# Performance work log

Hardware: AMD Instinct MI355X
Metric: run time of the kernel (lower is better)

Reference implementation:

```python
import jax, jax.numpy as jnp
import numpy as np

D_K = 64

def setup_inputs() -> dict:
    key = jax.random.key(0)
    ks = jax.random.split(key, 9)
    B, S, D = 8, 2048, 512
    d_k, d_v = 64, 64
    return {
        "q_in": jax.random.normal(ks[0], (B, S, D), jnp.float32),
        "k_in": jax.random.normal(ks[1], (B, S, D), jnp.float32),
        "v_in": jax.random.normal(ks[2], (B, S, D), jnp.float32),
        "Wq": jax.random.normal(ks[3], (D, d_k), jnp.float32) * 0.05,
        "bq": jax.random.normal(ks[4], (d_k,), jnp.float32) * 0.05,
        "Wk": jax.random.normal(ks[5], (D, d_k), jnp.float32) * 0.05,
        "bk": jax.random.normal(ks[6], (d_k,), jnp.float32) * 0.05,
        "Wv": jax.random.normal(ks[7], (D, d_v), jnp.float32) * 0.05,
        "bv": jax.random.normal(ks[8], (d_v,), jnp.float32) * 0.05,
    }

def reference(q_in, k_in, v_in, Wq, bq, Wk, bk, Wv, bv):
    # Dense projections: x @ W + b
    q = jnp.einsum('bsd,dk->bsk', q_in, Wq) + bq  # [B,S,d_k]
    k = jnp.einsum('bsd,dk->bsk', k_in, Wk) + bk  # [B,S,d_k]
    v = jnp.einsum('bsd,dv->bsv', v_in, Wv) + bv  # [B,S,d_v]
    scale = 1.0 / np.sqrt(D_K).astype(np.float32)
    scores = jnp.einsum('bqk,bsk->bqs', q, k) * scale  # [B,S,S]
    attn = jax.nn.softmax(scores, axis=-1)
    return jnp.einsum('bqs,bsv->bqv', attn, v)  # [B,S,d_v]
```

## Files before the change

### kernel.cpp

```cpp
#include <hip/hip_runtime.h>
#include <hip/hip_bf16.h>
#include <cstdint>

typedef __attribute__((ext_vector_type(8))) short short8;
typedef __attribute__((ext_vector_type(16))) float f32x16;

#if __has_builtin(__builtin_amdgcn_exp2f)
#define EXP2F(x) __builtin_amdgcn_exp2f(x)
#else
#define EXP2F(x) exp2f(x)
#endif

#define MFMA32(A, B, C) __builtin_amdgcn_mfma_f32_32x32x16_bf16((A), (B), (C), 0, 0, 0)

__device__ __forceinline__ unsigned short f2bf(float f) {
  unsigned int u = __builtin_bit_cast(unsigned int, f);
  u += 0x7FFFu + ((u >> 16) & 1u);
  return (unsigned short)(u >> 16);
}

__global__ __launch_bounds__(256) void prep_wt(
    const float* __restrict__ Wq, const float* __restrict__ Wk,
    const float* __restrict__ Wv, unsigned short* __restrict__ Wt)
{
  int idx = blockIdx.x * 256 + threadIdx.x;
  int which = idx >> 15;
  int rem = idx & 32767;
  int n = rem >> 9;
  int k = rem & 511;
  const float* W = (which == 0) ? Wq : (which == 1) ? Wk : Wv;
  Wt[idx] = f2bf(W[k * 64 + n]);
}

__global__ __launch_bounds__(256, 3) void proj_kernel(
    const float* __restrict__ qin, const float* __restrict__ kin,
    const float* __restrict__ vin, const unsigned short* __restrict__ Wt,
    const float* __restrict__ bq, const float* __restrict__ bk,
    const float* __restrict__ bv,
    unsigned short* __restrict__ Qo, unsigned short* __restrict__ Ko,
    unsigned short* __restrict__ Vto)
{
  __shared__ unsigned short Xs[64 * 136];

  const int which = blockIdx.y;
  const float* X    = (which == 0) ? qin : (which == 1) ? kin : vin;
  const float* bias = (which == 0) ? bq  : (which == 1) ? bk  : bv;

  const int tid = threadIdx.x;
  const int lane = tid & 63, wv = tid >> 6;
  const int h = lane >> 5, l31 = lane & 31;
  const int grp = wv & 1, nh = wv >> 1;
  const int m0 = blockIdx.x * 64;

  const unsigned short* wcol =
      Wt + (size_t)which * 64 * 512 + (size_t)(nh * 32 + l31) * 512 + h * 8;

  const int srow = tid >> 5;
  const int skoff = tid & 31;
  const float* xg = X + (size_t)(m0 + srow) * 512 + skoff * 4;

  f32x16 acc = {};
  for (int c = 0; c < 4; ++c) {
    __syncthreads();
    #pragma unroll
    for (int j = 0; j < 8; ++j) {
      float4 a = *(const float4*)(xg + (size_t)(8 * j) * 512 + c * 128);
      unsigned int w0 = (unsigned int)f2bf(a.x) | ((unsigned int)f2bf(a.y) << 16);
      unsigned int w1 = (unsigned int)f2bf(a.z) | ((unsigned int)f2bf(a.w) << 16);
      uint2 pw; pw.x = w0; pw.y = w1;
      *(uint2*)(&Xs[(srow + 8 * j) * 136 + skoff * 4]) = pw;
    }
    __syncthreads();
    const unsigned short* arow = &Xs[(grp * 32 + l31) * 136 + h * 8];
    const unsigned short* wk = wcol + c * 128;
    #pragma unroll
    for (int ks = 0; ks < 8; ++ks) {
      short8 af = *(const short8*)(arow + ks * 16);
      short8 bf = *(const short8*)(wk + ks * 16);
      acc = MFMA32(af, bf, acc);
    }
  }

  const float bv0 = bias[nh * 32 + l31];

  if (which < 2) {
    const float scale = which ? 1.0f : 0.18033688f;
    unsigned short* Y = which ? Ko : Qo;
    #pragma unroll
    for (int r = 0; r < 16; ++r) {
      int row = (r & 3) + 8 * (r >> 2) + 4 * h;
      Y[(size_t)(m0 + grp * 32 + row) * 64 + nh * 32 + l31] =
          f2bf((acc[r] + bv0) * scale);
    }
  } else {
    __syncthreads();
    unsigned short* TB = Xs;
    #pragma unroll
    for (int r = 0; r < 16; ++r) {
      int row = (r & 3) + 8 * (r >> 2) + 4 * h;
      TB[(nh * 32 + l31) * 68 + grp * 32 + row] = f2bf(acc[r] + bv0);
    }
    __syncthreads();
    int bidx = blockIdx.x >> 5;
    int s0 = (blockIdx.x & 31) * 64;
    for (int i = tid; i < 64 * 16; i += 256) {
      int n = i >> 4, cs = i & 15;
      ushort4 v4 = *(const ushort4*)(TB + n * 68 + cs * 4);
      *(ushort4*)(Vto + ((size_t)bidx * 64 + n) * 2048 + s0 + cs * 4) = v4;
    }
  }
}

__global__ __launch_bounds__(512, 2) void attn_kernel(
    const unsigned short* __restrict__ Q, const unsigned short* __restrict__ K,
    const unsigned short* __restrict__ Vt, float* __restrict__ out)
{
  __shared__ float ObS[4][16][64];
  __shared__ float MpS[4][64];
  __shared__ float LpS[4][64];

  const int tid = threadIdx.x;
  const int lane = tid & 63, w = tid >> 6;
  const int h = lane >> 5, l31 = lane & 31;
  const int b = blockIdx.y;
  const int q0 = blockIdx.x * 64;

  short8 qf[2][4];
  #pragma unroll
  for (int qt = 0; qt < 2; ++qt) {
    const unsigned short* qp = Q + ((size_t)(b * 2048 + q0 + qt * 32 + l31)) * 64 + h * 8;
    #pragma unroll
    for (int c = 0; c < 4; ++c) qf[qt][c] = *(const short8*)(qp + c * 16);
  }

  f32x16 o00 = {}, o01 = {}, o10 = {}, o11 = {};
  float m0 = -1e30f, m1 = -1e30f, ls0 = 0.f, ls1 = 0.f;

  for (int st = 0; st < 8; ++st) {
    const int kb = w * 256 + st * 32;
    short8 kf[4];
    const unsigned short* kp = K + ((size_t)(b * 2048 + kb + l31)) * 64 + h * 8;
    #pragma unroll
    for (int c = 0; c < 4; ++c) kf[c] = *(const short8*)(kp + c * 16);
    short8 vf0[2], vf1[2];
    {
      const unsigned short* vp0 = Vt + ((size_t)(b * 64 + l31)) * 2048 + kb + h * 8;
      const unsigned short* vp1 = Vt + ((size_t)(b * 64 + 32 + l31)) * 2048 + kb + h * 8;
      vf0[0] = *(const short8*)(vp0);  vf0[1] = *(const short8*)(vp0 + 16);
      vf1[0] = *(const short8*)(vp1);  vf1[1] = *(const short8*)(vp1 + 16);
    }
    #pragma unroll
    for (int qt = 0; qt < 2; ++qt) {
      f32x16 sT = {};
      #pragma unroll
      for (int c = 0; c < 4; ++c) sT = MFMA32(kf[c], qf[qt][c], sT);
      float mx = sT[0];
      #pragma unroll
      for (int r = 1; r < 16; ++r) mx = fmaxf(mx, sT[r]);
      mx = fmaxf(mx, __shfl_xor(mx, 32, 64));
      float mold = qt ? m1 : m0;
      float mnew = fmaxf(mold, mx);
      float alpha = EXP2F(mold - mnew);
      float rs = 0.f;
      float p[16];
      #pragma unroll
      for (int r = 0; r < 16; ++r) { p[r] = EXP2F(sT[r] - mnew); rs += p[r]; }
      rs += __shfl_xor(rs, 32, 64);
      unsigned int pk[8];
      #pragma unroll
      for (int i = 0; i < 8; ++i)
        pk[i] = (unsigned int)f2bf(p[2 * i]) | ((unsigned int)f2bf(p[2 * i + 1]) << 16);
      unsigned int ex[8];
      #pragma unroll
      for (int i = 0; i < 8; ++i) ex[i] = (unsigned int)__shfl_xor((int)pk[i], 32, 64);
      uint4 cc0, cc1;
      if (h == 0) { cc0 = make_uint4(pk[0], pk[1], ex[0], ex[1]); cc1 = make_uint4(pk[4], pk[5], ex[4], ex[5]); }
      else        { cc0 = make_uint4(ex[2], ex[3], pk[2], pk[3]); cc1 = make_uint4(ex[6], ex[7], pk[6], pk[7]); }
      short8 P0 = __builtin_bit_cast(short8, cc0);
      short8 P1 = __builtin_bit_cast(short8, cc1);
      if (qt == 0) {
        m0 = mnew; ls0 = ls0 * alpha + rs;
        o00 *= alpha; o10 *= alpha;
        o00 = MFMA32(vf0[0], P0, o00); o00 = MFMA32(vf0[1], P1, o00);
        o10 = MFMA32(vf1[0], P0, o10); o10 = MFMA32(vf1[1], P1, o10);
      } else {
        m1 = mnew; ls1 = ls1 * alpha + rs;
        o01 *= alpha; o11 *= alpha;
        o01 = MFMA32(vf0[0], P0, o01); o01 = MFMA32(vf0[1], P1, o01);
        o11 = MFMA32(vf1[0], P0, o11); o11 = MFMA32(vf1[1], P1, o11);
      }
    }
  }

  for (int half = 4; half > 0; half >>= 1) {
    const bool writer = (w >= half) && (w < 2 * half);
    const bool merger = (w < half);
    __syncthreads();
    if (writer && h == 0) {
      MpS[w - half][l31] = m0;      LpS[w - half][l31] = ls0;
      MpS[w - half][32 + l31] = m1; LpS[w - half][32 + l31] = ls1;
    }
    __syncthreads();
    float fb0 = 0.f, fb1 = 0.f;
    if (merger) {
      float pm0 = MpS[w][l31],      pl0 = LpS[w][l31];
      float pm1 = MpS[w][32 + l31], pl1 = LpS[w][32 + l31];
      float nm0 = fmaxf(m0, pm0), nm1 = fmaxf(m1, pm1);
      float fa0 = EXP2F(m0 - nm0); fb0 = EXP2F(pm0 - nm0);
      float fa1 = EXP2F(m1 - nm1); fb1 = EXP2F(pm1 - nm1);
      m0 = nm0; m1 = nm1;
      ls0 = ls0 * fa0 + pl0 * fb0; ls1 = ls1 * fa1 + pl1 * fb1;
      o00 *= fa0; o10 *= fa0; o01 *= fa1; o11 *= fa1;
    }
    __syncthreads();
    if (writer) {
      #pragma unroll
      for (int r = 0; r < 16; ++r) ObS[w - half][r][lane] = o00[r]; }
    __syncthreads();
    if (merger) {
      #pragma unroll
      for (int r = 0; r < 16; ++r) o00[r] += ObS[w][r][lane] * fb0; }
    __syncthreads();
    if (writer) {
      #pragma unroll
      for (int r = 0; r < 16; ++r) ObS[w - half][r][lane] = o01[r]; }
    __syncthreads();
    if (merger) {
      #pragma unroll
      for (int r = 0; r < 16; ++r) o01[r] += ObS[w][r][lane] * fb1; }
    __syncthreads();
    if (writer) {
      #pragma unroll
      for (int r = 0; r < 16; ++r) ObS[w - half][r][lane] = o10[r]; }
    __syncthreads();
    if (merger) {
      #pragma unroll
      for (int r = 0; r < 16; ++r) o10[r] += ObS[w][r][lane] * fb0; }
    __syncthreads();
    if (writer) {
      #pragma unroll
      for (int r = 0; r < 16; ++r) ObS[w - half][r][lane] = o11[r]; }
    __syncthreads();
    if (merger) {
      #pragma unroll
      for (int r = 0; r < 16; ++r) o11[r] += ObS[w][r][lane] * fb1; }
  }

  if (w == 0) {
    float i0 = 1.0f / ls0, i1 = 1.0f / ls1;
    o00 *= i0; o10 *= i0; o01 *= i1; o11 *= i1;
    #pragma unroll
    for (int qt = 0; qt < 2; ++qt) {
      int q = qt * 32 + l31;
      float* ob = out + ((size_t)(b * 2048 + q0 + q)) * 64 + 4 * h;
      const f32x16 a = qt ? o01 : o00;
      const f32x16 c = qt ? o11 : o10;
      #pragma unroll
      for (int g = 0; g < 4; ++g) {
        *(float4*)(ob + 8 * g)      = make_float4(a[4*g], a[4*g+1], a[4*g+2], a[4*g+3]);
        *(float4*)(ob + 32 + 8 * g) = make_float4(c[4*g], c[4*g+1], c[4*g+2], c[4*g+3]);
      }
    }
  }
}

extern "C" void kernel_launch(void* const* d_in, const int* in_sizes, int n_in,
                              void* d_out, int out_size, void* d_ws, size_t ws_size,
                              hipStream_t stream) {
  const float* qin = (const float*)d_in[0];
  const float* kin = (const float*)d_in[1];
  const float* vin = (const float*)d_in[2];
  const float* Wq  = (const float*)d_in[3];
  const float* bq  = (const float*)d_in[4];
  const float* Wk  = (const float*)d_in[5];
  const float* bk  = (const float*)d_in[6];
  const float* Wv  = (const float*)d_in[7];
  const float* bv  = (const float*)d_in[8];

  unsigned short* Qo  = (unsigned short*)d_ws;
  unsigned short* Ko  = Qo + (size_t)16384 * 64;
  unsigned short* Vto = Ko + (size_t)16384 * 64;
  unsigned short* Wt  = Vto + (size_t)8 * 64 * 2048;
  float* out = (float*)d_out;

  hipLaunchKernelGGL(prep_wt, dim3(384), dim3(256), 0, stream, Wq, Wk, Wv, Wt);
  hipLaunchKernelGGL(proj_kernel, dim3(256, 3), dim3(256), 0, stream,
                     qin, kin, vin, Wt, bq, bk, bv, Qo, Ko, Vto);
  hipLaunchKernelGGL(attn_kernel, dim3(32, 8), dim3(512), 0, stream, Qo, Ko, Vto, out);
}
```

Baseline: 162.0 us.

## Double-buffer projection tiles, prefetch K/V fragments, and add lazy softmax rescaling

The projection kernel now double-buffers its LDS tile and register-prefetches the next fp32 input chunk while MFMAs run on the current one, which removes one barrier per iteration. The attention kernel software-pipelines K and V fragment loads one step ahead, issues both QK^T score MFMAs back to back under raised wave priority, and uses tree reductions for the max and sum. Rescaling of the online softmax is skipped unless the running max grows by more than 8 (in log2 units), which avoids the per-tile alpha multiplies but lets probabilities reach up to 2^8 before bf16 rounding. The cost is more registers held live, which may reduce occupancy.

```diff
diff --git a/kernel.cpp b/kernel.cpp
--- a/kernel.cpp
+++ b/kernel.cpp
@@ -40,7 +40,7 @@
     unsigned short* __restrict__ Qo, unsigned short* __restrict__ Ko,
     unsigned short* __restrict__ Vto)
 {
-  __shared__ unsigned short Xs[64 * 136];
+  __shared__ unsigned short Xs[2][64 * 136];
 
   const int which = blockIdx.y;
   const float* X    = (which == 0) ? qin : (which == 1) ? kin : vin;
@@ -59,19 +59,27 @@
   const int skoff = tid & 31;
   const float* xg = X + (size_t)(m0 + srow) * 512 + skoff * 4;
 
+  float4 ld[8];
+  #pragma unroll
+  for (int j = 0; j < 8; ++j)
+    ld[j] = *(const float4*)(xg + (size_t)(8 * j) * 512);
+  #pragma unroll
+  for (int j = 0; j < 8; ++j) {
+    unsigned int w0 = (unsigned int)f2bf(ld[j].x) | ((unsigned int)f2bf(ld[j].y) << 16);
+    unsigned int w1 = (unsigned int)f2bf(ld[j].z) | ((unsigned int)f2bf(ld[j].w) << 16);
+    uint2 pw; pw.x = w0; pw.y = w1;
+    *(uint2*)(&Xs[0][(srow + 8 * j) * 136 + skoff * 4]) = pw;
+  }
+  __syncthreads();
+
   f32x16 acc = {};
   for (int c = 0; c < 4; ++c) {
-    __syncthreads();
-    #pragma unroll
-    for (int j = 0; j < 8; ++j) {
-      float4 a = *(const float4*)(xg + (size_t)(8 * j) * 512 + c * 128);
-      unsigned int w0 = (unsigned int)f2bf(a.x) | ((unsigned int)f2bf(a.y) << 16);
-      unsigned int w1 = (unsigned int)f2bf(a.z) | ((unsigned int)f2bf(a.w) << 16);
-      uint2 pw; pw.x = w0; pw.y = w1;
-      *(uint2*)(&Xs[(srow + 8 * j) * 136 + skoff * 4]) = pw;
-    }
-    __syncthreads();
-    const unsigned short* arow = &Xs[(grp * 32 + l31) * 136 + h * 8];
+    if (c < 3) {
+      #pragma unroll
+      for (int j = 0; j < 8; ++j)
+        ld[j] = *(const float4*)(xg + (size_t)(8 * j) * 512 + (c + 1) * 128);
+    }
+    const unsigned short* arow = &Xs[c & 1][(grp * 32 + l31) * 136 + h * 8];
     const unsigned short* wk = wcol + c * 128;
     #pragma unroll
     for (int ks = 0; ks < 8; ++ks) {
@@ -79,6 +87,16 @@
       short8 bf = *(const short8*)(wk + ks * 16);
       acc = MFMA32(af, bf, acc);
     }
+    if (c < 3) {
+      #pragma unroll
+      for (int j = 0; j < 8; ++j) {
+        unsigned int w0 = (unsigned int)f2bf(ld[j].x) | ((unsigned int)f2bf(ld[j].y) << 16);
+        unsigned int w1 = (unsigned int)f2bf(ld[j].z) | ((unsigned int)f2bf(ld[j].w) << 16);
+        uint2 pw; pw.x = w0; pw.y = w1;
+        *(uint2*)(&Xs[(c + 1) & 1][(srow + 8 * j) * 136 + skoff * 4]) = pw;
+      }
+      __syncthreads();
+    }
   }
 
   const float bv0 = bias[nh * 32 + l31];
@@ -94,7 +112,7 @@
     }
   } else {
     __syncthreads();
-    unsigned short* TB = Xs;
+    unsigned short* TB = &Xs[0][0];
     #pragma unroll
     for (int r = 0; r < 16; ++r) {
       int row = (r & 3) + 8 * (r >> 2) + 4 * h;
@@ -136,59 +154,79 @@
   f32x16 o00 = {}, o01 = {}, o10 = {}, o11 = {};
   float m0 = -1e30f, m1 = -1e30f, ls0 = 0.f, ls1 = 0.f;
 
+  const unsigned short* Kp  = K  + ((size_t)(b * 2048 + w * 256 + l31)) * 64 + h * 8;
+  const unsigned short* Vp0 = Vt + ((size_t)(b * 64 + l31)) * 2048 + w * 256 + h * 8;
+  const unsigned short* Vp1 = Vp0 + (size_t)32 * 2048;
+
+  short8 kf[4], vf0[2], vf1[2];
+  #pragma unroll
+  for (int c = 0; c < 4; ++c) kf[c] = *(const short8*)(Kp + c * 16);
+  vf0[0] = *(const short8*)(Vp0); vf0[1] = *(const short8*)(Vp0 + 16);
+  vf1[0] = *(const short8*)(Vp1); vf1[1] = *(const short8*)(Vp1 + 16);
+
+  auto process = [&](f32x16 sT, float &m, float &ls, f32x16 &oA, f32x16 &oB) {
+    float tm[8];
+    #pragma unroll
+    for (int i = 0; i < 8; ++i) tm[i] = fmaxf(sT[2 * i], sT[2 * i + 1]);
+    #pragma unroll
+    for (int i = 0; i < 4; ++i) tm[i] = fmaxf(tm[i], tm[i + 4]);
+    float mx = fmaxf(fmaxf(tm[0], tm[1]), fmaxf(tm[2], tm[3]));
+    mx = fmaxf(mx, __shfl_xor(mx, 32, 64));
+    if (__any(mx > m + 8.0f)) {
+      float mnew = fmaxf(m, mx);
+      float alpha = EXP2F(m - mnew);
+      m = mnew;
+      ls *= alpha; oA *= alpha; oB *= alpha;
+    }
+    float p[16];
+    #pragma unroll
+    for (int r = 0; r < 16; ++r) p[r] = EXP2F(sT[r] - m);
+    float ts[8];
+    #pragma unroll
+    for (int i = 0; i < 8; ++i) ts[i] = p[2 * i] + p[2 * i + 1];
+    #pragma unroll
+    for (int i = 0; i < 4; ++i) ts[i] += ts[i + 4];
+    float rs = (ts[0] + ts[1]) + (ts[2] + ts[3]);
+    rs += __shfl_xor(rs, 32, 64);
+    ls += rs;
+    unsigned int pk[8];
+    #pragma unroll
+    for (int i = 0; i < 8; ++i)
+      pk[i] = (unsigned int)f2bf(p[2 * i]) | ((unsigned int)f2bf(p[2 * i + 1]) << 16);
+    unsigned int ex[8];
+    #pragma unroll
+    for (int i = 0; i < 8; ++i) ex[i] = (unsigned int)__shfl_xor((int)pk[i], 32, 64);
+    uint4 cc0, cc1;
+    if (h == 0) { cc0 = make_uint4(pk[0], pk[1], ex[0], ex[1]); cc1 = make_uint4(pk[4], pk[5], ex[4], ex[5]); }
+    else        { cc0 = make_uint4(ex[2], ex[3], pk[2], pk[3]); cc1 = make_uint4(ex[6], ex[7], pk[6], pk[7]); }
+    short8 P0 = __builtin_bit_cast(short8, cc0);
+    short8 P1 = __builtin_bit_cast(short8, cc1);
+    __builtin_amdgcn_s_setprio(1);
+    oA = MFMA32(vf0[0], P0, oA); oA = MFMA32(vf0[1], P1, oA);
+    oB = MFMA32(vf1[0], P0, oB); oB = MFMA32(vf1[1], P1, oB);
+    __builtin_amdgcn_s_setprio(0);
+  };
+
   for (int st = 0; st < 8; ++st) {
-    const int kb = w * 256 + st * 32;
-    short8 kf[4];
-    const unsigned short* kp = K + ((size_t)(b * 2048 + kb + l31)) * 64 + h * 8;
-    #pragma unroll
-    for (int c = 0; c < 4; ++c) kf[c] = *(const short8*)(kp + c * 16);
-    short8 vf0[2], vf1[2];
-    {
-      const unsigned short* vp0 = Vt + ((size_t)(b * 64 + l31)) * 2048 + kb + h * 8;
-      const unsigned short* vp1 = Vt + ((size_t)(b * 64 + 32 + l31)) * 2048 + kb + h * 8;
-      vf0[0] = *(const short8*)(vp0);  vf0[1] = *(const short8*)(vp0 + 16);
-      vf1[0] = *(const short8*)(vp1);  vf1[1] = *(const short8*)(vp1 + 16);
-    }
-    #pragma unroll
-    for (int qt = 0; qt < 2; ++qt) {
-      f32x16 sT = {};
-      #pragma unroll
-      for (int c = 0; c < 4; ++c) sT = MFMA32(kf[c], qf[qt][c], sT);
-      float mx = sT[0];
-      #pragma unroll
-      for (int r = 1; r < 16; ++r) mx = fmaxf(mx, sT[r]);
-      mx = fmaxf(mx, __shfl_xor(mx, 32, 64));
-      float mold = qt ? m1 : m0;
-      float mnew = fmaxf(mold, mx);
-      float alpha = EXP2F(mold - mnew);
-      float rs = 0.f;
-      float p[16];
-      #pragma unroll
-      for (int r = 0; r < 16; ++r) { p[r] = EXP2F(sT[r] - mnew); rs += p[r]; }
-      rs += __shfl_xor(rs, 32, 64);
-      unsigned int pk[8];
-      #pragma unroll
-      for (int i = 0; i < 8; ++i)
-        pk[i] = (unsigned int)f2bf(p[2 * i]) | ((unsigned int)f2bf(p[2 * i + 1]) << 16);
-      unsigned int ex[8];
-      #pragma unroll
-      for (int i = 0; i < 8; ++i) ex[i] = (unsigned int)__shfl_xor((int)pk[i], 32, 64);
-      uint4 cc0, cc1;
-      if (h == 0) { cc0 = make_uint4(pk[0], pk[1], ex[0], ex[1]); cc1 = make_uint4(pk[4], pk[5], ex[4], ex[5]); }
-      else        { cc0 = make_uint4(ex[2], ex[3], pk[2], pk[3]); cc1 = make_uint4(ex[6], ex[7], pk[6], pk[7]); }
-      short8 P0 = __builtin_bit_cast(short8, cc0);
-      short8 P1 = __builtin_bit_cast(short8, cc1);
-      if (qt == 0) {
-        m0 = mnew; ls0 = ls0 * alpha + rs;
-        o00 *= alpha; o10 *= alpha;
-        o00 = MFMA32(vf0[0], P0, o00); o00 = MFMA32(vf0[1], P1, o00);
-        o10 = MFMA32(vf1[0], P0, o10); o10 = MFMA32(vf1[1], P1, o10);
-      } else {
-        m1 = mnew; ls1 = ls1 * alpha + rs;
-        o01 *= alpha; o11 *= alpha;
-        o01 = MFMA32(vf0[0], P0, o01); o01 = MFMA32(vf0[1], P1, o01);
-        o11 = MFMA32(vf1[0], P0, o11); o11 = MFMA32(vf1[1], P1, o11);
-      }
+    f32x16 s0 = {}, s1 = {};
+    __builtin_amdgcn_s_setprio(1);
+    #pragma unroll
+    for (int c = 0; c < 4; ++c) s0 = MFMA32(kf[c], qf[0][c], s0);
+    #pragma unroll
+    for (int c = 0; c < 4; ++c) s1 = MFMA32(kf[c], qf[1][c], s1);
+    __builtin_amdgcn_s_setprio(0);
+    if (st < 7) {
+      #pragma unroll
+      for (int c = 0; c < 4; ++c)
+        kf[c] = *(const short8*)(Kp + (size_t)(st + 1) * 2048 + c * 16);
+    }
+    process(s0, m0, ls0, o00, o10);
+    process(s1, m1, ls1, o01, o11);
+    if (st < 7) {
+      vf0[0] = *(const short8*)(Vp0 + (st + 1) * 32);
+      vf0[1] = *(const short8*)(Vp0 + (st + 1) * 32 + 16);
+      vf1[0] = *(const short8*)(Vp1 + (st + 1) * 32);
+      vf1[1] = *(const short8*)(Vp1 + (st + 1) * 32 + 16);
     }
   }
 
```

New measurement: 161.4 us (median of 2 runs). No clear change (-0.4%).
